# Optimization experiments

Measured on AMD Instinct MI355X. Metric: run time of the kernel, lower is better.

Reference implementation:

```python
import jax, jax.numpy as jnp
import numpy as np

B, T, D_MODEL, N_HEADS = 2, 2048, 1024, 16
HEAD_DIM = D_MODEL // N_HEADS
GN_EPS = 1e-5


def decay_gammas(n_heads):
    # gamma_h = 1 - 2^(-5 - h*(8/n_heads))
    h = jnp.arange(n_heads, dtype=jnp.float32)
    return 1.0 - jnp.power(2.0, -5.0 - h * (8.0 / n_heads))


def setup_inputs() -> dict:
    key = jax.random.key(0)
    ks = jax.random.split(key, 7)
    w_scale = 0.02
    return {
        "x": jax.random.normal(ks[0], (B, T, D_MODEL), dtype=jnp.float32),
        "Wq": jax.random.normal(ks[1], (D_MODEL, D_MODEL), dtype=jnp.float32) * w_scale,
        "Wk": jax.random.normal(ks[2], (D_MODEL, D_MODEL), dtype=jnp.float32) * w_scale,
        "Wv": jax.random.normal(ks[3], (D_MODEL, D_MODEL), dtype=jnp.float32) * w_scale,
        "Wo": jax.random.normal(ks[4], (D_MODEL, D_MODEL), dtype=jnp.float32) * w_scale,
        "gn_w": jnp.ones((D_MODEL,), dtype=jnp.float32),
        "gn_b": jnp.zeros((D_MODEL,), dtype=jnp.float32),
    }


def reference(x, Wq, Wk, Wv, Wo, gn_w, gn_b):
    Bx, Tx, C = x.shape
    H, D = N_HEADS, C // N_HEADS
    gammas = decay_gammas(H)  # (H,)

    def split_heads(y):
        return y.reshape(Bx, Tx, H, D).transpose(0, 2, 1, 3)  # (B,H,T,D)

    # torch Linear: y = x @ W.T
    Q = split_heads(x @ Wq.T)
    K = split_heads(x @ Wk.T)
    V = split_heads(x @ Wv.T)

    # causal decay mask D[h,i,j] = gamma_h^(i-j) if i>=j else 0
    idx = jnp.arange(Tx, dtype=jnp.float32)
    diff = idx[:, None] - idx[None, :]  # (T,T)
    mask = jnp.where(diff >= 0,
                     gammas[:, None, None] ** jnp.maximum(diff, 0.0),
                     0.0)  # (H,T,T)

    scores = jnp.einsum("bhtd,bhsd->bhts", Q, K) / jnp.sqrt(jnp.float32(D))
    scores = scores * mask[None]  # (B,H,T,T)
    out = jnp.einsum("bhts,bhsd->bhtd", scores, V)  # (B,H,T,D)
    y = out.transpose(0, 2, 1, 3).reshape(Bx, Tx, C)  # merge heads

    # GroupNorm(n_heads, d_model) applied on (B, C, T): normalizes over
    # (head_dim, T) per group per batch element.
    z = y.transpose(0, 2, 1).reshape(Bx, H, D, Tx)
    mu = z.mean(axis=(2, 3), keepdims=True)
    var = z.var(axis=(2, 3), keepdims=True)
    zn = (z - mu) * jax.lax.rsqrt(var + GN_EPS)
    zn = zn * gn_w.reshape(1, H, D, 1) + gn_b.reshape(1, H, D, 1)
    y = zn.reshape(Bx, C, Tx).transpose(0, 2, 1)  # (B,T,C)

    return y @ Wo.T
```

## Files before the change

kernel.cpp:

```cpp
#include <hip/hip_runtime.h>
#include <hip/hip_bf16.h>

typedef __attribute__((ext_vector_type(8))) short short8;
typedef __attribute__((ext_vector_type(4))) float float4v;
typedef __attribute__((ext_vector_type(16))) float float16v;
typedef unsigned short u16;
typedef unsigned long long ull;

#define KD 1024

__device__ __forceinline__ u16 f2b(float f) {
    __hip_bfloat16 h = __float2bfloat16(f);
    return __builtin_bit_cast(u16, h);
}
__device__ __forceinline__ float b2f(u16 u) {
    unsigned x = ((unsigned)u) << 16;
    return __builtin_bit_cast(float, x);
}
__device__ __forceinline__ float lg_gamma(int h) {
    float gamma = 1.0f - exp2f(-5.0f - 0.5f * (float)h);
    return log2f(gamma);
}

__device__ __forceinline__ void async_cp16(const u16* g, u16* l) {
    __builtin_amdgcn_global_load_lds(
        (const __attribute__((address_space(1))) void*)g,
        (__attribute__((address_space(3))) void*)l,
        16, 0, 0);
}

__global__ __launch_bounds__(256)
void cvt_all(const float* __restrict__ x, const float* __restrict__ wq,
             const float* __restrict__ wk, const float* __restrict__ wv,
             const float* __restrict__ wo,
             u16* __restrict__ xb, u16* __restrict__ wqkvb, u16* __restrict__ wob)
{
    int bid = blockIdx.x;
    if (bid < 4096) {
        long i = (long)bid * 1024 + threadIdx.x * 4;
        float4 v = *(const float4*)(x + i);
        ushort4 u;
        u.x = f2b(v.x); u.y = f2b(v.y); u.z = f2b(v.z); u.w = f2b(v.w);
        *(ushort4*)(xb + i) = u;
    } else {
        int wbid = bid - 4096;
        int mtx = wbid >> 10;
        int n = wbid & 1023;
        const float* src = (mtx == 0) ? wq : (mtx == 1) ? wk : (mtx == 2) ? wv : wo;
        u16* dst = (mtx == 3) ? wob : (wqkvb + (size_t)mtx * 1048576);
        float sc = (mtx == 0) ? 0.125f : 1.0f;
        int k0 = threadIdx.x * 4;
        float4 v = *(const float4*)(src + (size_t)n * 1024 + k0);
        int panel = n >> 5, row = n & 31, kg = k0 >> 4, kh = (k0 >> 3) & 1, off = k0 & 7;
        size_t o = (size_t)panel * 32768 + (size_t)kg * 512 + kh * 256 + row * 8 + off;
        ushort4 u;
        u.x = f2b(v.x * sc); u.y = f2b(v.y * sc); u.z = f2b(v.z * sc); u.w = f2b(v.w * sc);
        *(ushort4*)(dst + o) = u;
    }
}

template<int MODE>
__global__ __launch_bounds__(256)
void gemm_nt(const u16* __restrict__ A, const u16* __restrict__ Bpk,
             u16* __restrict__ oQ, u16* __restrict__ oK,
             u16* __restrict__ oKt, u16* __restrict__ oVt,
             float* __restrict__ of)
{
    constexpr int TM = (MODE == 0) ? 128 : 64;
    constexpr int MI = (MODE == 0) ? 2 : 1;
    __shared__ __attribute__((aligned(16))) u16 Sh[(MODE == 0) ? 16384 : 4096];
    u16* As = Sh;
    const int tid = threadIdx.x;
    const int lane = tid & 63;
    const int wv = tid >> 6;
    const int wm = wv >> 1, wn = wv & 1;
    const int row32 = lane & 31, khalf = lane >> 5;
    const int lrow = lane >> 3, lseg = lane & 7;
    const int lin = blockIdx.x + gridDim.x * blockIdx.y;
    const int xcd = lin & 7, idx = lin >> 3;
    int m_tile, n_tile;
    if (MODE == 0) { m_tile = (idx & 3) + 4 * xcd; n_tile = idx >> 2; }
    else           { m_tile = (idx & 7) + 8 * xcd; n_tile = idx >> 3; }
    const int m0 = m_tile * TM, n0 = n_tile * 128;

    float16v acc[MI][2];
#pragma unroll
    for (int i = 0; i < MI; i++)
#pragma unroll
        for (int j = 0; j < 2; j++)
#pragma unroll
            for (int r = 0; r < 16; r++) acc[i][j][r] = 0.f;

    const int scol = (lseg ^ lrow) << 3;
    const u16* bp = Bpk + (size_t)((n0 >> 5) + wn * 2) * 32768 + (size_t)lane * 8;

    for (int kt = 0; kt < KD; kt += 64) {
        __syncthreads();
#pragma unroll
        for (int i = 0; i < TM / 32; i++) {
            int r = wv * (TM / 4) + i * 8;
            async_cp16(A + (size_t)(m0 + r + lrow) * KD + kt + scol, &As[r * 64]);
        }
        short8 bgl[4][2];
#pragma unroll
        for (int ks = 0; ks < 4; ks++)
#pragma unroll
            for (int j = 0; j < 2; j++)
                bgl[ks][j] = *(const short8*)(bp + (size_t)j * 32768 + ((kt >> 4) + ks) * 512);
        __syncthreads();
#pragma unroll
        for (int ks = 0; ks < 4; ks++) {
            short8 af[MI];
#pragma unroll
            for (int i = 0; i < MI; i++) {
                int row = wm * (MI * 32) + i * 32 + row32;
                af[i] = *(const short8*)(&As[row * 64 + (((ks * 2 + khalf) ^ (row & 7)) << 3)]);
            }
#pragma unroll
            for (int i = 0; i < MI; i++)
#pragma unroll
                for (int j = 0; j < 2; j++)
                    acc[i][j] = __builtin_amdgcn_mfma_f32_32x32x16_bf16(af[i], bgl[ks][j], acc[i][j], 0, 0, 0);
        }
    }

    if (MODE == 0) {
        const int wsel = n0 >> 10;
        if (wsel <= 1) {
            u16* dst = (wsel == 0) ? oQ : oK;
#pragma unroll
            for (int i = 0; i < 2; i++)
#pragma unroll
                for (int j = 0; j < 2; j++) {
                    int gn = n0 + wn * 64 + j * 32 + row32;
                    int dd = gn & 63, hh = (gn >> 6) & 15;
#pragma unroll
                    for (int reg = 0; reg < 16; reg++) {
                        int m = m0 + wm * 64 + i * 32 + (reg & 3) + 8 * (reg >> 2) + 4 * khalf;
                        int b = m >> 11, t = m & 2047;
                        dst[(size_t)(b * 16 + hh) * 131072 + t * 64 + dd] = f2b(acc[i][j][reg]);
                    }
                }
        }
        if (wsel >= 1) {
            __syncthreads();
            u16* Tl = Sh + wv * 4096;
#pragma unroll
            for (int i = 0; i < 2; i++)
#pragma unroll
                for (int j = 0; j < 2; j++) {
                    int n_loc = j * 32 + row32;
#pragma unroll
                    for (int g = 0; g < 4; g++) {
                        int m4 = i * 32 + 8 * g + 4 * khalf;
                        ull pk = (ull)f2b(acc[i][j][4 * g]) | ((ull)f2b(acc[i][j][4 * g + 1]) << 16) |
                                 ((ull)f2b(acc[i][j][4 * g + 2]) << 32) | ((ull)f2b(acc[i][j][4 * g + 3]) << 48);
                        *(ull*)(&Tl[n_loc * 64 + (((m4 >> 3) ^ (n_loc & 7)) << 3) + (m4 & 7)]) = pk;
                    }
                }
            __syncthreads();
            int gnb = n0 + wn * 64;
            int hh = (gnb >> 6) & 15;
            int mb = m0 + wm * 64;
            int bh = (mb >> 11) * 16 + hh;
            int t0 = mb & 2047;
            u16* dstT = (wsel == 1) ? oKt : oVt;
            int rr = lane >> 3, ss = lane & 7;
#pragma unroll
            for (int g = 0; g < 8; g++) {
                int row = 8 * g + rr;
                short8 v = *(const short8*)(&Tl[row * 64 + ((ss ^ rr) << 3)]);
                *(short8*)(&dstT[(size_t)bh * 131072 + (size_t)row * 2048 + t0 + ss * 8]) = v;
            }
        }
    } else {
        int gn0 = n0 + wn * 64 + row32;
#pragma unroll
        for (int g = 0; g < 4; g++)
#pragma unroll
            for (int rr = 0; rr < 4; rr++) {
                int reg = 4 * g + rr;
                int m = m0 + wm * 32 + 8 * g + 4 * khalf + rr;
                of[(size_t)m * 1024 + gn0] = acc[0][0][reg];
                of[(size_t)m * 1024 + gn0 + 32] = acc[0][1][reg];
            }
    }
}

__global__ __launch_bounds__(256)
void chunk_state(const u16* __restrict__ Kt, const u16* __restrict__ Vt,
                 u16* __restrict__ U)
{
    const int c = blockIdx.x, bh = blockIdx.y, h = bh & 15;
    const int tid = threadIdx.x, lane = tid & 63, w = tid >> 6;
    const int row16 = lane & 15, quad = lane >> 4;
    const float lg = lg_gamma(h);
    const size_t base = (size_t)bh * 131072;

    float4v acc[4];
    float4v zero4 = {0.f, 0.f, 0.f, 0.f};
#pragma unroll
    for (int tn = 0; tn < 4; tn++) acc[tn] = zero4;

#pragma unroll
    for (int kb = 0; kb < 2; kb++) {
        short8 a = *(const short8*)(Vt + base + (size_t)(16 * w + row16) * 2048 + c * 64 + kb * 32 + quad * 8);
        short8 as;
        int e0 = 63 - (kb * 32 + quad * 8);
#pragma unroll
        for (int jj = 0; jj < 8; jj++) {
            float v = b2f((u16)a[jj]) * exp2f(lg * (float)(e0 - jj));
            as[jj] = (short)f2b(v);
        }
#pragma unroll
        for (int tn = 0; tn < 4; tn++) {
            short8 bfr = *(const short8*)(Kt + base + (size_t)(16 * tn + row16) * 2048 + c * 64 + kb * 32 + quad * 8);
            acc[tn] = __builtin_amdgcn_mfma_f32_16x16x32_bf16(as, bfr, acc[tn], 0, 0, 0);
        }
    }
    u16* up = U + ((size_t)bh * 32 + c) * 4096;
#pragma unroll
    for (int tn = 0; tn < 4; tn++)
#pragma unroll
        for (int r = 0; r < 4; r++)
            up[(16 * w + quad * 4 + r) * 64 + 16 * tn + row16] = f2b(acc[tn][r]);
}

__global__ __launch_bounds__(256)
void retention_chunk(const u16* __restrict__ Q, const u16* __restrict__ Kb,
                     const u16* __restrict__ Vt, const u16* __restrict__ U,
                     u16* __restrict__ Yb, float* __restrict__ stats)
{
    __shared__ __attribute__((aligned(16))) u16 Pl[4][16 * 72];
    __shared__ __attribute__((aligned(16))) u16 Sl[4096];
    __shared__ float red[8];
    const int c = blockIdx.x, bh = blockIdx.y, h = bh & 15;
    const int tid = threadIdx.x, lane = tid & 63, w = tid >> 6;
    const int row16 = lane & 15, quad = lane >> 4;
    const float lg = lg_gamma(h);
    const size_t base = (size_t)bh * 131072;
    float4v zero4 = {0.f, 0.f, 0.f, 0.f};

    short8 qf[2];
#pragma unroll
    for (int kb = 0; kb < 2; kb++)
        qf[kb] = *(const short8*)(Q + base + (size_t)(c * 64 + 16 * w + row16) * 64 + kb * 32 + quad * 8);

    if (c != 0) {
        const float g64 = exp2f(lg * 64.0f);
        float sreg[16];
#pragma unroll
        for (int j = 0; j < 16; j++) sreg[j] = 0.f;
        for (int cp = 0; cp < c; cp++) {
            const u16* up = U + ((size_t)bh * 32 + cp) * 4096 + tid * 8;
            short8 u0 = *(const short8*)(up);
            short8 u1 = *(const short8*)(up + 2048);
#pragma unroll
            for (int jj = 0; jj < 8; jj++) {
                sreg[jj]     = g64 * sreg[jj]     + b2f((u16)u0[jj]);
                sreg[8 + jj] = g64 * sreg[8 + jj] + b2f((u16)u1[jj]);
            }
        }
#pragma unroll
        for (int j = 0; j < 2; j++) {
            int e0 = j * 2048 + tid * 8;
            int row = e0 >> 6, col8 = (e0 >> 3) & 7;
            short8 pk;
#pragma unroll
            for (int jj = 0; jj < 8; jj++) pk[jj] = (short)f2b(sreg[j * 8 + jj]);
            *(short8*)(&Sl[row * 64 + ((col8 ^ (row & 7)) << 3)]) = pk;
        }
    }

    float4v accp[4];
#pragma unroll
    for (int tn = 0; tn < 4; tn++) accp[tn] = zero4;
#pragma unroll
    for (int tn = 0; tn < 4; tn++)
#pragma unroll
        for (int kb = 0; kb < 2; kb++) {
            short8 kf = *(const short8*)(Kb + base + (size_t)(c * 64 + 16 * tn + row16) * 64 + kb * 32 + quad * 8);
            accp[tn] = __builtin_amdgcn_mfma_f32_16x16x32_bf16(qf[kb], kf, accp[tn], 0, 0, 0);
        }
#pragma unroll
    for (int tn = 0; tn < 4; tn++)
#pragma unroll
        for (int r = 0; r < 4; r++) {
            int a_loc = 16 * w + quad * 4 + r;
            int b_loc = 16 * tn + row16;
            int d = a_loc - b_loc;
            float v = (d >= 0) ? accp[tn][r] * exp2f(lg * (float)d) : 0.f;
            Pl[w][(quad * 4 + r) * 72 + b_loc] = f2b(v);
        }
    __syncthreads();

    short8 pf[2];
#pragma unroll
    for (int kb = 0; kb < 2; kb++)
        pf[kb] = *(const short8*)(&Pl[w][row16 * 72 + kb * 32 + quad * 8]);

    float4v acco[4], acci[4];
#pragma unroll
    for (int tn = 0; tn < 4; tn++) { acco[tn] = zero4; acci[tn] = zero4; }
#pragma unroll
    for (int tn = 0; tn < 4; tn++)
#pragma unroll
        for (int kb = 0; kb < 2; kb++) {
            short8 vf = *(const short8*)(Vt + base + (size_t)(16 * tn + row16) * 2048 + c * 64 + kb * 32 + quad * 8);
            acco[tn] = __builtin_amdgcn_mfma_f32_16x16x32_bf16(pf[kb], vf, acco[tn], 0, 0, 0);
            if (c != 0) {
                int srow = 16 * tn + row16, scol8 = kb * 4 + quad;
                short8 sf = *(const short8*)(&Sl[srow * 64 + ((scol8 ^ (srow & 7)) << 3)]);
                acci[tn] = __builtin_amdgcn_mfma_f32_16x16x32_bf16(qf[kb], sf, acci[tn], 0, 0, 0);
            }
        }

    const int b = bh >> 4;
    float s = 0.f, s2 = 0.f;
#pragma unroll
    for (int tn = 0; tn < 4; tn++)
#pragma unroll
        for (int r = 0; r < 4; r++) {
            int a_loc = 16 * w + quad * 4 + r;
            float gi = exp2f(lg * (float)(a_loc + 1));
            int t = c * 64 + a_loc, d2 = 16 * tn + row16;
            float yv = acco[tn][r] + gi * acci[tn][r];
            u16 yq = f2b(yv);
            Yb[((size_t)(b * 2048 + t)) * 1024 + h * 64 + d2] = yq;
            float yr = b2f(yq);
            s += yr;
            s2 += yr * yr;
        }
#pragma unroll
    for (int off = 32; off; off >>= 1) {
        s += __shfl_down(s, off, 64);
        s2 += __shfl_down(s2, off, 64);
    }
    if (lane == 0) { red[w] = s; red[4 + w] = s2; }
    __syncthreads();
    if (tid == 0) {
        atomicAdd(&stats[2 * bh], red[0] + red[1] + red[2] + red[3]);
        atomicAdd(&stats[2 * bh + 1], red[4] + red[5] + red[6] + red[7]);
    }
}

__global__ __launch_bounds__(256)
void gn_apply(u16* __restrict__ Z, const float* __restrict__ stats,
              const float* __restrict__ gnw, const float* __restrict__ gnb)
{
    int i8 = (blockIdx.x * 256 + threadIdx.x) * 8;
    int b = i8 >> 21, cc = i8 & 1023;
    int bh = b * 16 + (cc >> 6);
    short8 v = *(const short8*)(Z + i8);
    float S = stats[2 * bh], S2 = stats[2 * bh + 1];
    float mu = S * (1.0f / 131072.f);
    float var = S2 * (1.0f / 131072.f) - mu * mu;
    float rsg = rsqrtf(var + 1e-5f);
    float4 w0 = *(const float4*)(gnw + cc);
    float4 w1 = *(const float4*)(gnw + cc + 4);
    float4 b0 = *(const float4*)(gnb + cc);
    float4 b1 = *(const float4*)(gnb + cc + 4);
    short8 o;
    o[0] = (short)f2b((b2f((u16)v[0]) - mu) * rsg * w0.x + b0.x);
    o[1] = (short)f2b((b2f((u16)v[1]) - mu) * rsg * w0.y + b0.y);
    o[2] = (short)f2b((b2f((u16)v[2]) - mu) * rsg * w0.z + b0.z);
    o[3] = (short)f2b((b2f((u16)v[3]) - mu) * rsg * w0.w + b0.w);
    o[4] = (short)f2b((b2f((u16)v[4]) - mu) * rsg * w1.x + b1.x);
    o[5] = (short)f2b((b2f((u16)v[5]) - mu) * rsg * w1.y + b1.y);
    o[6] = (short)f2b((b2f((u16)v[6]) - mu) * rsg * w1.z + b1.z);
    o[7] = (short)f2b((b2f((u16)v[7]) - mu) * rsg * w1.w + b1.w);
    *(short8*)(Z + i8) = o;
}

extern "C" void kernel_launch(void* const* d_in, const int* in_sizes, int n_in,
                              void* d_out, int out_size, void* d_ws, size_t ws_size,
                              hipStream_t stream) {
    const float* x   = (const float*)d_in[0];
    const float* Wq  = (const float*)d_in[1];
    const float* Wk  = (const float*)d_in[2];
    const float* Wv  = (const float*)d_in[3];
    const float* Wo  = (const float*)d_in[4];
    const float* gnw = (const float*)d_in[5];
    const float* gnb = (const float*)d_in[6];
    float* out = (float*)d_out;
    char* ws = (char*)d_ws;

    u16*  xb    = (u16*)(ws + 0);
    u16*  wqkvb = (u16*)(ws + 8388608);
    u16*  wob   = (u16*)(ws + 14680064);
    u16*  Qs    = (u16*)(ws + 16777216);
    u16*  Kb    = (u16*)(ws + 25165824);
    u16*  Kt    = (u16*)(ws + 33554432);
    u16*  Vt    = (u16*)(ws + 41943040);
    u16*  U     = (u16*)(ws + 50331648);
    u16*  Yb    = (u16*)(ws + 67108864);
    float* stats= (float*)(ws + 100663296);

    hipMemsetAsync(stats, 0, 64 * sizeof(float), stream);

    cvt_all<<<8192, 256, 0, stream>>>(x, Wq, Wk, Wv, Wo, xb, wqkvb, wob);

    gemm_nt<0><<<dim3(24, 32), 256, 0, stream>>>(xb, wqkvb, Qs, Kb, Kt, Vt, nullptr);

    chunk_state<<<dim3(32, 32), 256, 0, stream>>>(Kt, Vt, U);
    retention_chunk<<<dim3(32, 32), 256, 0, stream>>>(Qs, Kb, Vt, U, Yb, stats);

    gn_apply<<<2048, 256, 0, stream>>>(Yb, stats, gnw, gnb);

    gemm_nt<1><<<dim3(8, 64), 256, 0, stream>>>(Yb, wob, nullptr, nullptr, nullptr, nullptr, out);
}
```

Measured before the change: 180.8 us.

## Double-buffer A tiles and B registers in projection GEMM k-loop

```diff
diff --git a/kernel.cpp b/kernel.cpp
--- a/kernel.cpp
+++ b/kernel.cpp
@@ -68,8 +68,10 @@
 {
     constexpr int TM = (MODE == 0) ? 128 : 64;
     constexpr int MI = (MODE == 0) ? 2 : 1;
-    __shared__ __attribute__((aligned(16))) u16 Sh[(MODE == 0) ? 16384 : 4096];
-    u16* As = Sh;
+    constexpr int AHALF = TM * 64;
+    __shared__ __attribute__((aligned(16))) u16 Sh[2 * AHALF];
+    u16* As0 = Sh;
+    u16* As1 = Sh + AHALF;
     const int tid = threadIdx.x;
     const int lane = tid & 63;
     const int wv = tid >> 6;
@@ -94,27 +96,28 @@
     const int scol = (lseg ^ lrow) << 3;
     const u16* bp = Bpk + (size_t)((n0 >> 5) + wn * 2) * 32768 + (size_t)lane * 8;
 
-    for (int kt = 0; kt < KD; kt += 64) {
-        __syncthreads();
+    auto stage = [&](u16* dstb, int kt) {
 #pragma unroll
         for (int i = 0; i < TM / 32; i++) {
             int r = wv * (TM / 4) + i * 8;
-            async_cp16(A + (size_t)(m0 + r + lrow) * KD + kt + scol, &As[r * 64]);
-        }
-        short8 bgl[4][2];
+            async_cp16(A + (size_t)(m0 + r + lrow) * KD + kt + scol, &dstb[r * 64]);
+        }
+    };
+    auto loadB = [&](short8 (&bgl)[4][2], int kt) {
 #pragma unroll
         for (int ks = 0; ks < 4; ks++)
 #pragma unroll
             for (int j = 0; j < 2; j++)
                 bgl[ks][j] = *(const short8*)(bp + (size_t)j * 32768 + ((kt >> 4) + ks) * 512);
-        __syncthreads();
+    };
+    auto compute = [&](const u16* Asb, short8 (&bgl)[4][2]) {
 #pragma unroll
         for (int ks = 0; ks < 4; ks++) {
             short8 af[MI];
 #pragma unroll
             for (int i = 0; i < MI; i++) {
                 int row = wm * (MI * 32) + i * 32 + row32;
-                af[i] = *(const short8*)(&As[row * 64 + (((ks * 2 + khalf) ^ (row & 7)) << 3)]);
+                af[i] = *(const short8*)(&Asb[row * 64 + (((ks * 2 + khalf) ^ (row & 7)) << 3)]);
             }
 #pragma unroll
             for (int i = 0; i < MI; i++)
@@ -122,6 +125,30 @@
                 for (int j = 0; j < 2; j++)
                     acc[i][j] = __builtin_amdgcn_mfma_f32_32x32x16_bf16(af[i], bgl[ks][j], acc[i][j], 0, 0, 0);
         }
+    };
+
+    short8 bglA[4][2], bglB[4][2];
+    stage(As0, 0);
+    loadB(bglA, 0);
+    for (int kt = 0; kt < KD; kt += 128) {
+        __builtin_amdgcn_s_barrier();
+        stage(As1, kt + 64);
+        loadB(bglB, kt + 64);
+        if constexpr (MODE == 0) asm volatile("s_waitcnt vmcnt(12)" ::: "memory");
+        else                     asm volatile("s_waitcnt vmcnt(10)" ::: "memory");
+        __builtin_amdgcn_s_barrier();
+        compute(As0, bglA);
+        __builtin_amdgcn_s_barrier();
+        if (kt + 128 < KD) {
+            stage(As0, kt + 128);
+            loadB(bglA, kt + 128);
+            if constexpr (MODE == 0) asm volatile("s_waitcnt vmcnt(12)" ::: "memory");
+            else                     asm volatile("s_waitcnt vmcnt(10)" ::: "memory");
+        } else {
+            asm volatile("s_waitcnt vmcnt(0)" ::: "memory");
+        }
+        __builtin_amdgcn_s_barrier();
+        compute(As1, bglB);
     }
 
     if (MODE == 0) {
```

Measured after the change: 182.6 us. Within noise of the previous version (+1.0%).

## Fold GroupNorm into per-batch Wo weights and bias, drop gn_apply pass

Applied to the files above, without the earlier changes.

```diff
diff --git a/kernel.cpp b/kernel.cpp
--- a/kernel.cpp
+++ b/kernel.cpp
@@ -32,8 +32,7 @@
 __global__ __launch_bounds__(256)
 void cvt_all(const float* __restrict__ x, const float* __restrict__ wq,
              const float* __restrict__ wk, const float* __restrict__ wv,
-             const float* __restrict__ wo,
-             u16* __restrict__ xb, u16* __restrict__ wqkvb, u16* __restrict__ wob)
+             u16* __restrict__ xb, u16* __restrict__ wqkvb)
 {
     int bid = blockIdx.x;
     if (bid < 4096) {
@@ -44,18 +43,26 @@
         *(ushort4*)(xb + i) = u;
     } else {
         int wbid = bid - 4096;
-        int mtx = wbid >> 10;
-        int n = wbid & 1023;
-        const float* src = (mtx == 0) ? wq : (mtx == 1) ? wk : (mtx == 2) ? wv : wo;
-        u16* dst = (mtx == 3) ? wob : (wqkvb + (size_t)mtx * 1048576);
+        int mtx = wbid >> 5;
+        int panel = wbid & 31;
+        const float* src = (mtx == 0) ? wq : (mtx == 1) ? wk : wv;
+        u16* dst = wqkvb + (size_t)mtx * 1048576 + (size_t)panel * 32768;
         float sc = (mtx == 0) ? 0.125f : 1.0f;
-        int k0 = threadIdx.x * 4;
-        float4 v = *(const float4*)(src + (size_t)n * 1024 + k0);
-        int panel = n >> 5, row = n & 31, kg = k0 >> 4, kh = (k0 >> 3) & 1, off = k0 & 7;
-        size_t o = (size_t)panel * 32768 + (size_t)kg * 512 + kh * 256 + row * 8 + off;
-        ushort4 u;
-        u.x = f2b(v.x * sc); u.y = f2b(v.y * sc); u.z = f2b(v.z * sc); u.w = f2b(v.w * sc);
-        *(ushort4*)(dst + o) = u;
+        int lane = threadIdx.x & 63, wvid = threadIdx.x >> 6;
+        int row = lane & 31, kh = lane >> 5;
+        const float* srow = src + (size_t)(panel * 32 + row) * 1024 + kh * 8;
+#pragma unroll
+        for (int i = 0; i < 16; i++) {
+            int kg = i * 4 + wvid;
+            float4 a = *(const float4*)(srow + kg * 16);
+            float4 b = *(const float4*)(srow + kg * 16 + 4);
+            short8 o;
+            o[0] = (short)f2b(a.x * sc); o[1] = (short)f2b(a.y * sc);
+            o[2] = (short)f2b(a.z * sc); o[3] = (short)f2b(a.w * sc);
+            o[4] = (short)f2b(b.x * sc); o[5] = (short)f2b(b.y * sc);
+            o[6] = (short)f2b(b.z * sc); o[7] = (short)f2b(b.w * sc);
+            *(short8*)(dst + kg * 512 + lane * 8) = o;
+        }
     }
 }
 
@@ -64,7 +71,7 @@
 void gemm_nt(const u16* __restrict__ A, const u16* __restrict__ Bpk,
              u16* __restrict__ oQ, u16* __restrict__ oK,
              u16* __restrict__ oKt, u16* __restrict__ oVt,
-             float* __restrict__ of)
+             float* __restrict__ of, const float* __restrict__ bias)
 {
     constexpr int TM = (MODE == 0) ? 128 : 64;
     constexpr int MI = (MODE == 0) ? 2 : 1;
@@ -92,7 +99,8 @@
             for (int r = 0; r < 16; r++) acc[i][j][r] = 0.f;
 
     const int scol = (lseg ^ lrow) << 3;
-    const u16* bp = Bpk + (size_t)((n0 >> 5) + wn * 2) * 32768 + (size_t)lane * 8;
+    const u16* bp = Bpk + ((MODE == 1) ? (size_t)(m0 >> 11) * 1048576 : 0)
+                  + (size_t)((n0 >> 5) + wn * 2) * 32768 + (size_t)lane * 8;
 
     for (int kt = 0; kt < KD; kt += 64) {
         __syncthreads();
@@ -175,14 +183,16 @@
         }
     } else {
         int gn0 = n0 + wn * 64 + row32;
+        float bv0 = bias[(m0 >> 11) * 1024 + gn0];
+        float bv1 = bias[(m0 >> 11) * 1024 + gn0 + 32];
 #pragma unroll
         for (int g = 0; g < 4; g++)
 #pragma unroll
             for (int rr = 0; rr < 4; rr++) {
                 int reg = 4 * g + rr;
                 int m = m0 + wm * 32 + 8 * g + 4 * khalf + rr;
-                of[(size_t)m * 1024 + gn0] = acc[0][0][reg];
-                of[(size_t)m * 1024 + gn0 + 32] = acc[0][1][reg];
+                of[(size_t)m * 1024 + gn0] = acc[0][0][reg] + bv0;
+                of[(size_t)m * 1024 + gn0 + 32] = acc[0][1][reg] + bv1;
             }
     }
 }
@@ -345,31 +355,58 @@
 }
 
 __global__ __launch_bounds__(256)
-void gn_apply(u16* __restrict__ Z, const float* __restrict__ stats,
-              const float* __restrict__ gnw, const float* __restrict__ gnb)
+void gn_fold(const float* __restrict__ wo, const float* __restrict__ stats,
+             const float* __restrict__ gnw, const float* __restrict__ gnb,
+             u16* __restrict__ wob2, float* __restrict__ bias)
 {
-    int i8 = (blockIdx.x * 256 + threadIdx.x) * 8;
-    int b = i8 >> 21, cc = i8 & 1023;
-    int bh = b * 16 + (cc >> 6);
-    short8 v = *(const short8*)(Z + i8);
-    float S = stats[2 * bh], S2 = stats[2 * bh + 1];
-    float mu = S * (1.0f / 131072.f);
-    float var = S2 * (1.0f / 131072.f) - mu * mu;
-    float rsg = rsqrtf(var + 1e-5f);
-    float4 w0 = *(const float4*)(gnw + cc);
-    float4 w1 = *(const float4*)(gnw + cc + 4);
-    float4 b0 = *(const float4*)(gnb + cc);
-    float4 b1 = *(const float4*)(gnb + cc + 4);
-    short8 o;
-    o[0] = (short)f2b((b2f((u16)v[0]) - mu) * rsg * w0.x + b0.x);
-    o[1] = (short)f2b((b2f((u16)v[1]) - mu) * rsg * w0.y + b0.y);
-    o[2] = (short)f2b((b2f((u16)v[2]) - mu) * rsg * w0.z + b0.z);
-    o[3] = (short)f2b((b2f((u16)v[3]) - mu) * rsg * w0.w + b0.w);
-    o[4] = (short)f2b((b2f((u16)v[4]) - mu) * rsg * w1.x + b1.x);
-    o[5] = (short)f2b((b2f((u16)v[5]) - mu) * rsg * w1.y + b1.y);
-    o[6] = (short)f2b((b2f((u16)v[6]) - mu) * rsg * w1.z + b1.z);
-    o[7] = (short)f2b((b2f((u16)v[7]) - mu) * rsg * w1.w + b1.w);
-    *(short8*)(Z + i8) = o;
+    int bid = blockIdx.x;
+    if (bid < 32) {
+        int panel = bid;
+        int lane = threadIdx.x & 63, wvid = threadIdx.x >> 6;
+        int row = lane & 31, kh = lane >> 5;
+        const float* srow = wo + (size_t)(panel * 32 + row) * 1024 + kh * 8;
+#pragma unroll
+        for (int i = 0; i < 16; i++) {
+            int kg = i * 4 + wvid;
+            int c0 = kg * 16 + kh * 8;
+            int hh = c0 >> 6;
+            float4 a = *(const float4*)(srow + kg * 16);
+            float4 b = *(const float4*)(srow + kg * 16 + 4);
+            float4 w0 = *(const float4*)(gnw + c0);
+            float4 w1 = *(const float4*)(gnw + c0 + 4);
+            size_t off = (size_t)panel * 32768 + kg * 512 + lane * 8;
+#pragma unroll
+            for (int bb = 0; bb < 2; bb++) {
+                int bh = bb * 16 + hh;
+                float S = stats[2 * bh], S2 = stats[2 * bh + 1];
+                float mu = S * (1.0f / 131072.f);
+                float rsg = rsqrtf(S2 * (1.0f / 131072.f) - mu * mu + 1e-5f);
+                short8 o;
+                o[0] = (short)f2b(a.x * rsg * w0.x); o[1] = (short)f2b(a.y * rsg * w0.y);
+                o[2] = (short)f2b(a.z * rsg * w0.z); o[3] = (short)f2b(a.w * rsg * w0.w);
+                o[4] = (short)f2b(b.x * rsg * w1.x); o[5] = (short)f2b(b.y * rsg * w1.y);
+                o[6] = (short)f2b(b.z * rsg * w1.z); o[7] = (short)f2b(b.w * rsg * w1.w);
+                *(short8*)(wob2 + (size_t)bb * 1048576 + off) = o;
+            }
+        }
+    } else {
+        int t = (bid - 32) * 256 + threadIdx.x;
+        int bb = t >> 10, n = t & 1023;
+        const float* wrow = wo + (size_t)n * 1024;
+        float acc = 0.f;
+        for (int c = 0; c < 1024; c += 4) {
+            int bh = bb * 16 + (c >> 6);
+            float S = stats[2 * bh], S2 = stats[2 * bh + 1];
+            float mu = S * (1.0f / 131072.f);
+            float rsg = rsqrtf(S2 * (1.0f / 131072.f) - mu * mu + 1e-5f);
+            float4 wo4 = *(const float4*)(wrow + c);
+            float4 w4 = *(const float4*)(gnw + c);
+            float4 b4 = *(const float4*)(gnb + c);
+            acc += (b4.x - mu * rsg * w4.x) * wo4.x + (b4.y - mu * rsg * w4.y) * wo4.y
+                 + (b4.z - mu * rsg * w4.z) * wo4.z + (b4.w - mu * rsg * w4.w) * wo4.w;
+        }
+        bias[t] = acc;
+    }
 }
 
 extern "C" void kernel_launch(void* const* d_in, const int* in_sizes, int n_in,
@@ -387,25 +424,26 @@
 
     u16*  xb    = (u16*)(ws + 0);
     u16*  wqkvb = (u16*)(ws + 8388608);
-    u16*  wob   = (u16*)(ws + 14680064);
     u16*  Qs    = (u16*)(ws + 16777216);
     u16*  Kb    = (u16*)(ws + 25165824);
     u16*  Kt    = (u16*)(ws + 33554432);
     u16*  Vt    = (u16*)(ws + 41943040);
     u16*  U     = (u16*)(ws + 50331648);
     u16*  Yb    = (u16*)(ws + 67108864);
+    u16*  wob2  = (u16*)(ws + 75497472);
+    float* bias = (float*)(ws + 79691776);
     float* stats= (float*)(ws + 100663296);
 
     hipMemsetAsync(stats, 0, 64 * sizeof(float), stream);
 
-    cvt_all<<<8192, 256, 0, stream>>>(x, Wq, Wk, Wv, Wo, xb, wqkvb, wob);
-
-    gemm_nt<0><<<dim3(24, 32), 256, 0, stream>>>(xb, wqkvb, Qs, Kb, Kt, Vt, nullptr);
+    cvt_all<<<4192, 256, 0, stream>>>(x, Wq, Wk, Wv, xb, wqkvb);
+
+    gemm_nt<0><<<dim3(24, 32), 256, 0, stream>>>(xb, wqkvb, Qs, Kb, Kt, Vt, nullptr, nullptr);
 
     chunk_state<<<dim3(32, 32), 256, 0, stream>>>(Kt, Vt, U);
     retention_chunk<<<dim3(32, 32), 256, 0, stream>>>(Qs, Kb, Vt, U, Yb, stats);
 
-    gn_apply<<<2048, 256, 0, stream>>>(Yb, stats, gnw, gnb);
-
-    gemm_nt<1><<<dim3(8, 64), 256, 0, stream>>>(Yb, wob, nullptr, nullptr, nullptr, nullptr, out);
-}
+    gn_fold<<<40, 256, 0, stream>>>(Wo, stats, gnw, gnb, wob2, bias);
+
+    gemm_nt<1><<<dim3(8, 64), 256, 0, stream>>>(Yb, wob2, nullptr, nullptr, nullptr, nullptr, out, bias);
+}
```

Result: slower. 213.7 us (+18.2%).
